# Performance work log

Measured on AMD Instinct MI355X. Metric: run time of the kernel, lower is better.

Reference implementation:

```python
import jax, jax.numpy as jnp
import numpy as np


def setup_inputs() -> dict:
    key = jax.random.key(0)
    k1, k2, k3, k4, k5 = jax.random.split(key, 5)
    B, T, U, D = 4, 256, 64, 512
    H, V = 512, 1024  # forward_output_size, num_classes
    return {
        "encoder_outputs": jax.random.normal(k1, (B, T, D), dtype=jnp.float32),
        "decoder_outputs": jax.random.normal(k2, (B, U, D), dtype=jnp.float32),
        "w1": jax.random.normal(k3, (H, 2 * D), dtype=jnp.float32) * 0.02,
        "b1": jax.random.normal(k4, (H,), dtype=jnp.float32) * 0.02,
        "w2": jax.random.normal(k5, (V, H), dtype=jnp.float32) * 0.02,
    }


def reference(encoder_outputs, decoder_outputs, w1, b1, w2):
    # Faithful to: concat([enc broadcast to (B,T,U,D), dec broadcast to (B,T,U,D)], -1)
    # -> Linear(w1,b1) -> GELU(tanh) -> Linear(w2, no bias).
    # Linear on the concat equals split-weight projections summed via broadcast
    # (classic RNNT joint decomposition): same math, avoids the (B,T,U,2D) tensor.
    D = encoder_outputs.shape[-1]
    w_enc, w_dec = w1[:, :D], w1[:, D:]
    enc_proj = jnp.einsum("btd,hd->bth", encoder_outputs, w_enc)  # (B,T,H)
    dec_proj = jnp.einsum("bud,hd->buh", decoder_outputs, w_dec)  # (B,U,H)
    hidden = enc_proj[:, :, None, :] + dec_proj[:, None, :, :] + b1  # (B,T,U,H)
    hidden = jax.nn.gelu(hidden, approximate=True)  # tanh approximation, matches nn.GELU('tanh')
    logits = jnp.einsum("btuh,vh->btuv", hidden, w2)  # (B,T,U,V)
    return logits
```

## Files before the change

### kernel.cpp

```cpp
#include <hip/hip_runtime.h>
#include <hip/hip_bf16.h>
#include <stdint.h>


typedef __bf16 bf16_t;
typedef bf16_t bf16x8 __attribute__((ext_vector_type(8)));
typedef float f32x4 __attribute__((ext_vector_type(4)));
typedef unsigned short u16x8 __attribute__((ext_vector_type(8)));

#define GLD16(gp, lp)                                                          \
  __builtin_amdgcn_global_load_lds(                                            \
      (const __attribute__((address_space(1))) void*)(gp),                     \
      (__attribute__((address_space(3))) void*)(lp), 16, 0, 0)

__device__ __forceinline__ unsigned short f2bf(float f) {
  unsigned int u = __float_as_uint(f);
  return (unsigned short)((u + 0x7FFFu + ((u >> 16) & 1u)) >> 16);
}

__device__ __forceinline__ float gelu_f(float x) {
  float t = 1.5957691216057308f * x + 0.07135481283867141f * (x * x * x);
  float e = __expf(-t);
  return x * __builtin_amdgcn_rcpf(1.0f + e);
}

__global__ __launch_bounds__(256) void prep_kernel(
    const float* __restrict__ enc, const float* __restrict__ dec,
    const float* __restrict__ w1, const float* __restrict__ w2,
    unsigned short* __restrict__ o) {
  int i = (blockIdx.x * 256 + threadIdx.x) * 4;
  float4 v;
  if (i < 524288) {
    v = *(const float4*)(enc + i);
  } else if (i < 655360) {
    v = *(const float4*)(dec + (i - 524288));
  } else if (i < 917504) {
    int j = i - 655360;
    v = *(const float4*)(w1 + (j >> 9) * 1024 + (j & 511));
  } else if (i < 1179648) {
    int j = i - 917504;
    v = *(const float4*)(w1 + (j >> 9) * 1024 + 512 + (j & 511));
  } else {
    v = *(const float4*)(w2 + (i - 1179648));
  }
  ushort4 r;
  r.x = f2bf(v.x); r.y = f2bf(v.y); r.z = f2bf(v.z); r.w = f2bf(v.w);
  *(ushort4*)(o + i) = r;
}

__global__ __launch_bounds__(256) void hidden_kernel(
    const float* __restrict__ ep, const float* __restrict__ dp,
    const float* __restrict__ b1, unsigned short* __restrict__ o) {
  int g = blockIdx.x * 256 + threadIdx.x;
  int m = g >> 6;
  int h = (g & 63) << 3;
  int er = m >> 6;
  int dr = ((m >> 14) << 6) | (m & 63);
  float4 e0 = *(const float4*)(ep + er * 512 + h);
  float4 e1 = *(const float4*)(ep + er * 512 + h + 4);
  float4 d0 = *(const float4*)(dp + dr * 512 + h);
  float4 d1 = *(const float4*)(dp + dr * 512 + h + 4);
  float4 b0 = *(const float4*)(b1 + h);
  float4 b1v = *(const float4*)(b1 + h + 4);
  u16x8 r;
  r[0] = f2bf(gelu_f(e0.x + d0.x + b0.x));
  r[1] = f2bf(gelu_f(e0.y + d0.y + b0.y));
  r[2] = f2bf(gelu_f(e0.z + d0.z + b0.z));
  r[3] = f2bf(gelu_f(e0.w + d0.w + b0.w));
  r[4] = f2bf(gelu_f(e1.x + d1.x + b1v.x));
  r[5] = f2bf(gelu_f(e1.y + d1.y + b1v.y));
  r[6] = f2bf(gelu_f(e1.z + d1.z + b1v.z));
  r[7] = f2bf(gelu_f(e1.w + d1.w + b1v.w));
  *(u16x8*)(o + (size_t)g * 8) = r;
}

__device__ __forceinline__ void gemm_core(
    const bf16_t* __restrict__ A, const bf16_t* __restrict__ B,
    float* __restrict__ C, int m0, int n0, int N, int K) {
  __shared__ bf16_t sA[128 * 64];
  __shared__ bf16_t sB[128 * 64];

  const int tid = threadIdx.x;
  const int lane = tid & 63;
  const int w = tid >> 6;
  const int wm = (w >> 1) * 64;
  const int wn = (w & 1) * 64;

  const int srow = w * 32 + (lane >> 3);
  const int scol = (((lane & 7) ^ (lane >> 3)) << 3);
  const bf16_t* gA = A + (size_t)(m0 + srow) * K + scol;
  const bf16_t* gB = B + (size_t)(n0 + srow) * K + scol;

  const int rowA = wm + (lane & 15);
  const int rowB = wn + (lane & 15);
  const int sw0 = (lane >> 4) ^ (lane & 7);
  const bf16x8* pA = (const bf16x8*)sA;
  const bf16x8* pB = (const bf16x8*)sB;

  f32x4 acc[4][4] = {};

  for (int kt = 0; kt < K; kt += 64) {
#pragma unroll
    for (int j = 0; j < 4; j++) {
      GLD16(gA + (size_t)(j * 8) * K + kt, sA + (w * 4 + j) * 512);
      GLD16(gB + (size_t)(j * 8) * K + kt, sB + (w * 4 + j) * 512);
    }
    __syncthreads();

#pragma unroll
    for (int kk = 0; kk < 2; kk++) {
      const int sw = sw0 ^ (kk << 2);
      bf16x8 af[4], bb[4];
#pragma unroll
      for (int i = 0; i < 4; i++) af[i] = pA[(rowA + i * 16) * 8 + sw];
#pragma unroll
      for (int j = 0; j < 4; j++) bb[j] = pB[(rowB + j * 16) * 8 + sw];
#pragma unroll
      for (int i = 0; i < 4; i++)
#pragma unroll
        for (int j = 0; j < 4; j++)
          acc[i][j] = __builtin_amdgcn_mfma_f32_16x16x32_bf16(
              af[i], bb[j], acc[i][j], 0, 0, 0);
    }
    __syncthreads();
  }

  const int crow = m0 + wm + (lane >> 4) * 4;
  const int ccol = n0 + wn + (lane & 15);
  float* Cp = C + (size_t)crow * N + ccol;
#pragma unroll
  for (int i = 0; i < 4; i++)
#pragma unroll
    for (int r = 0; r < 4; r++)
#pragma unroll
      for (int j = 0; j < 4; j++)
        Cp[(size_t)(i * 16 + r) * N + j * 16] = acc[i][j][r];
}

__global__ __launch_bounds__(256) void gemm_big(
    const bf16_t* __restrict__ A, const bf16_t* __restrict__ B,
    float* __restrict__ C, int M, int N, int K) {
  gemm_core(A, B, C, blockIdx.y * 128, blockIdx.x * 128, N, K);
}

__global__ __launch_bounds__(256) void proj_kernel(
    const bf16_t* __restrict__ encA, const bf16_t* __restrict__ wenc,
    float* __restrict__ encC, const bf16_t* __restrict__ decA,
    const bf16_t* __restrict__ wdec, float* __restrict__ decC) {
  int by = blockIdx.y;
  if (by < 8) {
    gemm_core(encA, wenc, encC, by * 128, blockIdx.x * 128, 512, 512);
  } else {
    gemm_core(decA, wdec, decC, (by - 8) * 128, blockIdx.x * 128, 512, 512);
  }
}

extern "C" void kernel_launch(void* const* d_in, const int* in_sizes, int n_in,
                              void* d_out, int out_size, void* d_ws,
                              size_t ws_size, hipStream_t stream) {
  const float* enc = (const float*)d_in[0];
  const float* dec = (const float*)d_in[1];
  const float* w1  = (const float*)d_in[2];
  const float* b1  = (const float*)d_in[3];
  const float* w2  = (const float*)d_in[4];
  float* out = (float*)d_out;

  unsigned short* bf      = (unsigned short*)d_ws;
  unsigned short* ws_enc  = bf;
  unsigned short* ws_dec  = bf + 524288;
  unsigned short* ws_wenc = bf + 655360;
  unsigned short* ws_wdec = bf + 917504;
  unsigned short* ws_w2   = bf + 1179648;
  float* encp = (float*)((char*)d_ws + 3407872);
  float* decp = encp + 524288;
  unsigned short* hid = (unsigned short*)(decp + 131072);

  prep_kernel<<<1664, 256, 0, stream>>>(enc, dec, w1, w2, bf);

  proj_kernel<<<dim3(4, 10), 256, 0, stream>>>(
      (const bf16_t*)ws_enc, (const bf16_t*)ws_wenc, encp,
      (const bf16_t*)ws_dec, (const bf16_t*)ws_wdec, decp);

  hidden_kernel<<<16384, 256, 0, stream>>>(encp, decp, b1, hid);

  gemm_big<<<dim3(8, 512), 256, 0, stream>>>(
      (const bf16_t*)hid, (const bf16_t*)ws_w2, out, 65536, 1024, 512);
}
```

Measured before the change: 380.7 us.

## Replace output GEMM with 256x256 double-buffered pipelined MFMA kernel

Replaces the 128x128 single-buffered output GEMM with a 256x256-tile, 512-thread kernel that double-buffers LDS and interleaves global-to-LDS staging with MFMA phases, using explicit vmcnt waits, barriers and s_setprio. It also swizzles the block index for L2 reuse. The aim is to hide load latency and raise MFMA utilisation. The cost is higher register and LDS pressure and hardcoded shapes.

```diff
diff --git a/kernel.cpp b/kernel.cpp
--- a/kernel.cpp
+++ b/kernel.cpp
@@ -137,12 +137,6 @@
         Cp[(size_t)(i * 16 + r) * N + j * 16] = acc[i][j][r];
 }
 
-__global__ __launch_bounds__(256) void gemm_big(
-    const bf16_t* __restrict__ A, const bf16_t* __restrict__ B,
-    float* __restrict__ C, int M, int N, int K) {
-  gemm_core(A, B, C, blockIdx.y * 128, blockIdx.x * 128, N, K);
-}
-
 __global__ __launch_bounds__(256) void proj_kernel(
     const bf16_t* __restrict__ encA, const bf16_t* __restrict__ wenc,
     float* __restrict__ encC, const bf16_t* __restrict__ decA,
@@ -155,6 +149,137 @@
   }
 }
 
+
+#define STG_A(BUF, RH, KT)                                                     \
+  do {                                                                         \
+    GLD16(gA + (size_t)((RH) * 64) * 512 + (KT) * 64,                          \
+          &sA[BUF][(RH) * 64 + w * 8][0]);                                     \
+    GLD16(gA + (size_t)((RH) * 64 + 128) * 512 + (KT) * 64,                    \
+          &sA[BUF][(RH) * 64 + 128 + w * 8][0]);                               \
+  } while (0)
+
+#define STG_B(BUF, H, KT)                                                      \
+  do {                                                                         \
+    GLD16(gB + (size_t)((H) * 128) * 512 + (KT) * 64,                          \
+          &sB[BUF][(H) * 128 + w * 16][0]);                                    \
+    GLD16(gB + (size_t)((H) * 128 + 8) * 512 + (KT) * 64,                      \
+          &sB[BUF][(H) * 128 + w * 16 + 8][0]);                                \
+  } while (0)
+
+#define RD_A(BUF, F, KK)                                                       \
+  pA[(BUF) * 2048 + (rowA + (F) * 16) * 8 + (sw0 ^ ((KK) << 2))]
+#define RD_B(BUF, ROFF, KK)                                                    \
+  pB[(BUF) * 2048 + (rowB + (ROFF)) * 8 + (sw0 ^ ((KK) << 2))]
+
+#define VMC4 asm volatile("s_waitcnt vmcnt(4)" ::: "memory")
+#define VMC0 asm volatile("s_waitcnt vmcnt(0)" ::: "memory")
+#define NOPX ((void)0)
+
+#define PHASE(BUF, RH, CH, STAGE, VM)                                          \
+  do {                                                                         \
+    if ((CH) == 0) {                                                           \
+      _Pragma("unroll") for (int f = 0; f < 4; f++) {                          \
+        af[f][0] = RD_A(BUF, (RH) * 4 + f, 0);                                 \
+        af[f][1] = RD_A(BUF, (RH) * 4 + f, 1);                                 \
+      }                                                                        \
+    }                                                                          \
+    _Pragma("unroll") for (int cf = 0; cf < 2; cf++) {                         \
+      bb[cf][0] = RD_B(BUF, (CH) * 128 + cf * 16, 0);                          \
+      bb[cf][1] = RD_B(BUF, (CH) * 128 + cf * 16, 1);                          \
+    }                                                                          \
+    STAGE;                                                                     \
+    VM;                                                                        \
+    __builtin_amdgcn_s_barrier();                                              \
+    __builtin_amdgcn_s_setprio(1);                                             \
+    _Pragma("unroll") for (int f = 0; f < 4; f++) {                            \
+      _Pragma("unroll") for (int cf = 0; cf < 2; cf++) {                       \
+        acc[(RH) * 4 + f][(CH) * 2 + cf] =                                     \
+            __builtin_amdgcn_mfma_f32_16x16x32_bf16(                           \
+                af[f][0], bb[cf][0], acc[(RH) * 4 + f][(CH) * 2 + cf], 0, 0,   \
+                0);                                                            \
+        acc[(RH) * 4 + f][(CH) * 2 + cf] =                                     \
+            __builtin_amdgcn_mfma_f32_16x16x32_bf16(                           \
+                af[f][1], bb[cf][1], acc[(RH) * 4 + f][(CH) * 2 + cf], 0, 0,   \
+                0);                                                            \
+      }                                                                        \
+    }                                                                          \
+    __builtin_amdgcn_s_setprio(0);                                             \
+    __builtin_amdgcn_s_barrier();                                              \
+  } while (0)
+
+__global__ __launch_bounds__(512, 2) void gemm_big2(
+    const bf16_t* __restrict__ A, const bf16_t* __restrict__ B,
+    float* __restrict__ C) {
+  __shared__ bf16_t sA[2][256][64];
+  __shared__ bf16_t sB[2][256][64];
+
+  const int tid = threadIdx.x;
+  const int lane = tid & 63;
+  const int w = tid >> 6;
+  const int wr = w >> 2;
+  const int wc = w & 3;
+
+  const int bid = blockIdx.x;
+  const int swz = (bid & 7) * 128 + (bid >> 3);
+  const int m0 = (swz >> 2) * 256;
+  const int n0 = (swz & 3) * 256;
+
+  const int srowA = w * 8 + (lane >> 3);
+  const int srowB = w * 16 + (lane >> 3);
+  const int scol = ((lane & 7) ^ (lane >> 3)) << 3;
+  const bf16_t* gA = A + (size_t)(m0 + srowA) * 512 + scol;
+  const bf16_t* gB = B + (size_t)(n0 + srowB) * 512 + scol;
+
+  const int rowA = wr * 128 + (lane & 15);
+  const int rowB = wc * 32 + (lane & 15);
+  const int sw0 = (lane >> 4) ^ (lane & 7);
+  const bf16x8* pA = (const bf16x8*)sA;
+  const bf16x8* pB = (const bf16x8*)sB;
+
+  f32x4 acc[8][4] = {};
+  bf16x8 af[4][2], bb[2][2];
+
+  STG_A(0, 0, 0); STG_B(0, 0, 0); STG_A(0, 1, 0); STG_B(0, 1, 0);
+  STG_A(1, 0, 1); STG_B(1, 0, 1);
+  VMC4;
+  __builtin_amdgcn_s_barrier();
+
+#pragma unroll 1
+  for (int i = 0; i < 3; i++) {
+    const int t1k = 2 * i + 1;
+    const int t2k = 2 * i + 2;
+    const int t3k = 2 * i + 3;
+    PHASE(0, 0, 0, STG_A(1, 1, t1k), NOPX);
+    PHASE(0, 0, 1, STG_B(1, 1, t1k), NOPX);
+    PHASE(0, 1, 0, STG_A(0, 0, t2k), NOPX);
+    PHASE(0, 1, 1, STG_B(0, 0, t2k), VMC4);
+    PHASE(1, 0, 0, STG_A(0, 1, t2k), NOPX);
+    PHASE(1, 0, 1, STG_B(0, 1, t2k), NOPX);
+    PHASE(1, 1, 0, STG_A(1, 0, t3k), NOPX);
+    PHASE(1, 1, 1, STG_B(1, 0, t3k), VMC4);
+  }
+  PHASE(0, 0, 0, STG_A(1, 1, 7), NOPX);
+  PHASE(0, 0, 1, STG_B(1, 1, 7), NOPX);
+  PHASE(0, 1, 0, NOPX, NOPX);
+  PHASE(0, 1, 1, NOPX, VMC0);
+  PHASE(1, 0, 0, NOPX, NOPX);
+  PHASE(1, 0, 1, NOPX, NOPX);
+  PHASE(1, 1, 0, NOPX, NOPX);
+  PHASE(1, 1, 1, NOPX, NOPX);
+
+  const int crow = m0 + wr * 128 + (lane >> 4) * 4;
+  const int ccol = n0 + wc * 32 + (lane & 15);
+  float* Cp = C + (size_t)crow * 1024 + ccol;
+#pragma unroll
+  for (int f = 0; f < 8; f++)
+#pragma unroll
+    for (int r = 0; r < 4; r++)
+#pragma unroll
+      for (int c = 0; c < 4; c++)
+        Cp[(size_t)(f * 16 + r) * 1024 + (c >> 1) * 128 + (c & 1) * 16] =
+            acc[f][c][r];
+}
+
 extern "C" void kernel_launch(void* const* d_in, const int* in_sizes, int n_in,
                               void* d_out, int out_size, void* d_ws,
                               size_t ws_size, hipStream_t stream) {
@@ -183,6 +308,6 @@
 
   hidden_kernel<<<16384, 256, 0, stream>>>(encp, decp, b1, hid);
 
-  gemm_big<<<dim3(8, 512), 256, 0, stream>>>(
-      (const bf16_t*)hid, (const bf16_t*)ws_w2, out, 65536, 1024, 512);
-}
+  gemm_big2<<<1024, 512, 0, stream>>>(
+      (const bf16_t*)hid, (const bf16_t*)ws_w2, out);
+}
```

Measured after the change: 362.4 us. 1.05x faster.
